# Kernel tuning notes

Measured on AMD Instinct MI355X. Metric: run time of the kernel, lower is better.

## Reference

```python
import jax, jax.numpy as jnp
import numpy as np


def setup_inputs() -> dict:
    key = jax.random.key(0)
    k1, k2 = jax.random.split(key)
    B, C, H, W = 16, 3, 512, 512
    predicted = jax.random.normal(k1, (B, C, H, W), dtype=jnp.float32)
    target = jax.random.randint(k2, (B, H, W), 0, 3, dtype=jnp.int32)
    return {"predicted": predicted, "target": target, "num_classes": 3}


def reference(predicted, target, num_classes):
    # predicted: [B, C, H, W] logits; target: [B, H, W] int labels
    B, C, H, W = predicted.shape
    smooth = 1.0

    # F.cross_entropy with default 'mean' reduction over all pixels
    logp = jax.nn.log_softmax(predicted, axis=1)           # [B,C,H,W]
    ce = -jnp.mean(jnp.take_along_axis(logp, target[:, None, :, :], axis=1))

    # Dice: the original casts softmax probs with .long() before summing,
    # which truncates toward zero (probs in [0,1) -> 0, exactly 1.0 -> 1).
    # We reproduce that faithfully with jnp.trunc.
    probs = jnp.exp(logp).reshape(B, C, H * W)             # softmax probs, [B,C,HW]
    tp = jnp.trunc(probs)                                   # faithful to .long() cast
    tgt = target.reshape(B, H * W)
    onehot = (tgt[:, None, :] == jnp.arange(num_classes)[None, :, None]).astype(probs.dtype)  # [B,nc,HW]

    intersection = jnp.sum(tp[:, :num_classes, :] * onehot, axis=-1)                 # [B,nc]
    union = jnp.sum(tp[:, :num_classes, :], axis=-1) + jnp.sum(onehot, axis=-1)      # [B,nc]
    coef = (2.0 * intersection + smooth) / (union + smooth)                           # [B,nc]
    batch_dice = jnp.mean(coef)  # mean over classes then batch == mean over both

    return ce + 1.0 - batch_dice
```

## Files before the change

kernel.cpp:

```cpp
#include <hip/hip_runtime.h>

constexpr int B_   = 16;
constexpr int C_   = 3;
constexpr int HW_  = 512 * 512;
constexpr int THREADS = 256;
constexpr int BLOCKS_PER_IMG = 128;
constexpr int NBLOCKS = B_ * BLOCKS_PER_IMG;
constexpr int F4_PER_BLOCK = HW_ / 4 / BLOCKS_PER_IMG;
constexpr int ITERS = F4_PER_BLOCK / THREADS;
constexpr int REC = 8;


__global__ __launch_bounds__(THREADS) void dice_ce_partial(
    const float* __restrict__ pred, const int* __restrict__ tgt,
    float* __restrict__ ws) {
  const int b = blockIdx.x / BLOCKS_PER_IMG;
  const int j = blockIdx.x % BLOCKS_PER_IMG;
  const int t = threadIdx.x;

  const float4* p0 = (const float4*)(pred + (size_t)b * C_ * HW_);
  const float4* p1 = (const float4*)(pred + (size_t)b * C_ * HW_ + HW_);
  const float4* p2 = (const float4*)(pred + (size_t)b * C_ * HW_ + 2 * HW_);
  const int4*   tg = (const int4*)(tgt + (size_t)b * HW_);

  float4 A0[ITERS], A1[ITERS], A2[ITERS];
  int4   T[ITERS];
#pragma unroll
  for (int i = 0; i < ITERS; ++i) {
    const int idx = j * F4_PER_BLOCK + i * THREADS + t;
    A0[i] = p0[idx];
    A1[i] = p1[idx];
    A2[i] = p2[idx];
    T[i]  = tg[idx];
  }

  float ce = 0.f;
  int pkA = 0, pkB = 0, pkC = 0, pkD = 0;

#pragma unroll
  for (int i = 0; i < ITERS; ++i) {
    float x0s[4] = {A0[i].x, A0[i].y, A0[i].z, A0[i].w};
    float x1s[4] = {A1[i].x, A1[i].y, A1[i].z, A1[i].w};
    float x2s[4] = {A2[i].x, A2[i].y, A2[i].z, A2[i].w};
    int   tvs[4] = {T[i].x, T[i].y, T[i].z, T[i].w};
#pragma unroll
    for (int k = 0; k < 4; ++k) {
      float x0 = x0s[k], x1 = x1s[k], x2 = x2s[k];
      int tv = tvs[k];
      float m  = fmaxf(x0, fmaxf(x1, x2));
      float e0 = __expf(x0 - m), e1 = __expf(x1 - m), e2 = __expf(x2 - m);
      float s  = e0 + e1 + e2;
      float ls = __logf(s);
      float xt = (tv == 0) ? x0 : ((tv == 1) ? x1 : x2);
      ce += (m + ls) - xt;
      int t0 = (e0 >= s) ? 1 : 0;
      int t1 = (e1 >= s) ? 1 : 0;
      int t2 = (e2 >= s) ? 1 : 0;
      pkA += ((tv == 1) ? 1 : 0) + ((tv == 2) ? (1 << 16) : 0);
      pkB += t0 + (t1 << 16);
      pkC += t2 + (((tv == 0) ? t0 : 0) << 16);
      pkD += ((tv == 1) ? t1 : 0) + (((tv == 2) ? t2 : 0) << 16);
    }
  }

  int pks[4] = {pkA, pkB, pkC, pkD};
#pragma unroll
  for (int off = 32; off > 0; off >>= 1) {
    ce += __shfl_down(ce, off, 64);
#pragma unroll
    for (int k = 0; k < 4; ++k) pks[k] += __shfl_down(pks[k], off, 64);
  }

  __shared__ float ceR[THREADS / 64];
  __shared__ int   pkR[THREADS / 64][4];
  const int wave = t >> 6, lane = t & 63;
  if (lane == 0) {
    ceR[wave] = ce;
#pragma unroll
    for (int k = 0; k < 4; ++k) pkR[wave][k] = pks[k];
  }
  __syncthreads();
  if (t == 0) {
#pragma unroll
    for (int w = 1; w < THREADS / 64; ++w) {
      ce += ceR[w];
#pragma unroll
      for (int k = 0; k < 4; ++k) pks[k] += pkR[w][k];
    }
    float4* rec = (float4*)(ws + (size_t)blockIdx.x * REC);
    rec[0] = make_float4(ce, __int_as_float(pks[0]), __int_as_float(pks[1]),
                         __int_as_float(pks[2]));
    rec[1] = make_float4(__int_as_float(pks[3]), 0.f, 0.f, 0.f);
  }
}

__global__ __launch_bounds__(1024) void dice_ce_final(
    const float* __restrict__ ws, float* __restrict__ out) {
  const int t = threadIdx.x;
  const int img = t >> 6;
  const int lane = t & 63;

  float ce = 0.f;
  float cnt1 = 0.f, cnt2 = 0.f;
  float tps0 = 0.f, tps1 = 0.f, tps2 = 0.f;
  float itr0 = 0.f, itr1 = 0.f, itr2 = 0.f;
#pragma unroll
  for (int r = 0; r < 2; ++r) {
    const int idx = img * BLOCKS_PER_IMG + r * 64 + lane;
    const float4* rec = (const float4*)(ws + (size_t)idx * REC);
    float4 r0 = rec[0], r1 = rec[1];
    ce += r0.x;
    int pA = __float_as_int(r0.y), pB = __float_as_int(r0.z);
    int pC = __float_as_int(r0.w), pD = __float_as_int(r1.x);
    cnt1 += (float)(pA & 0xffff); cnt2 += (float)(pA >> 16);
    tps0 += (float)(pB & 0xffff); tps1 += (float)(pB >> 16);
    tps2 += (float)(pC & 0xffff); itr0 += (float)(pC >> 16);
    itr1 += (float)(pD & 0xffff); itr2 += (float)(pD >> 16);
  }
  float v[9] = {ce, cnt1, cnt2, tps0, tps1, tps2, itr0, itr1, itr2};
#pragma unroll
  for (int k = 0; k < 9; ++k) {
#pragma unroll
    for (int off = 32; off > 0; off >>= 1) v[k] += __shfl_down(v[k], off, 64);
  }

  __shared__ float ceS[16];
  __shared__ float coefS[16];
  if (lane == 0) {
    float c1 = v[1], c2 = v[2];
    float c0 = (float)HW_ - c1 - c2;
    float coef = (2.f * v[6] + 1.f) / (v[3] + c0 + 1.f)
               + (2.f * v[7] + 1.f) / (v[4] + c1 + 1.f)
               + (2.f * v[8] + 1.f) / (v[5] + c2 + 1.f);
    ceS[img] = v[0];
    coefS[img] = coef;
  }
  __syncthreads();
  if (t == 0) {
    float cesum = 0.f, cf = 0.f;
#pragma unroll
    for (int i = 0; i < 16; ++i) { cesum += ceS[i]; cf += coefS[i]; }
    out[0] = cesum / ((float)B_ * (float)HW_) + 1.f - cf / (float)(B_ * C_);
  }
}

extern "C" void kernel_launch(void* const* d_in, const int* in_sizes, int n_in,
                              void* d_out, int out_size, void* d_ws, size_t ws_size,
                              hipStream_t stream) {
  const float* pred = (const float*)d_in[0];
  const int*   tgt  = (const int*)d_in[1];
  float*       out  = (float*)d_out;
  float*       ws   = (float*)d_ws;

  dice_ce_partial<<<NBLOCKS, THREADS, 0, stream>>>(pred, tgt, ws);
  dice_ce_final<<<1, 1024, 0, stream>>>(ws, out);
}
```

Baseline: 96.94 us.

## Fuse final reduction into partial kernel via last-block atomic counter

Replaces the separate single-block finalize kernel with a last-block-done pattern: each block publishes its record, fences, and increments a global counter, and the block that finishes last performs the cross-image reduction and writes the output. This removes one kernel launch and its gap but adds a hipMemsetAsync to reset the counter, an atomic per block, and a serial tail reduction done by only 256 threads. The memset is itself a stream operation, so the launch savings may be partly offset.

```diff
diff --git a/kernel.cpp b/kernel.cpp
--- a/kernel.cpp
+++ b/kernel.cpp
@@ -10,10 +10,11 @@
 constexpr int ITERS = F4_PER_BLOCK / THREADS;
 constexpr int REC = 8;
 
+constexpr size_t CNT_OFF_FLOATS = (size_t)NBLOCKS * REC;
 
-__global__ __launch_bounds__(THREADS) void dice_ce_partial(
+__global__ __launch_bounds__(THREADS) void dice_ce_fused(
     const float* __restrict__ pred, const int* __restrict__ tgt,
-    float* __restrict__ ws) {
+    float* __restrict__ ws, float* __restrict__ out) {
   const int b = blockIdx.x / BLOCKS_PER_IMG;
   const int j = blockIdx.x % BLOCKS_PER_IMG;
   const int t = threadIdx.x;
@@ -73,6 +74,9 @@
 
   __shared__ float ceR[THREADS / 64];
   __shared__ int   pkR[THREADS / 64][4];
+  __shared__ int   lastFlag;
+  __shared__ float ceS[B_];
+  __shared__ float coefS[B_];
   const int wave = t >> 6, lane = t & 63;
   if (lane == 0) {
     ceR[wave] = ce;
@@ -91,55 +95,58 @@
     rec[0] = make_float4(ce, __int_as_float(pks[0]), __int_as_float(pks[1]),
                          __int_as_float(pks[2]));
     rec[1] = make_float4(__int_as_float(pks[3]), 0.f, 0.f, 0.f);
+    __threadfence();
+    unsigned int old =
+        atomicAdd((unsigned int*)(ws + CNT_OFF_FLOATS), 1u);
+    lastFlag = (old == (unsigned int)(NBLOCKS - 1)) ? 1 : 0;
   }
-}
+  __syncthreads();
+  if (lastFlag == 0) return;
 
-__global__ __launch_bounds__(1024) void dice_ce_final(
-    const float* __restrict__ ws, float* __restrict__ out) {
-  const int t = threadIdx.x;
-  const int img = t >> 6;
-  const int lane = t & 63;
+  __threadfence();
 
-  float ce = 0.f;
-  float cnt1 = 0.f, cnt2 = 0.f;
-  float tps0 = 0.f, tps1 = 0.f, tps2 = 0.f;
-  float itr0 = 0.f, itr1 = 0.f, itr2 = 0.f;
 #pragma unroll
-  for (int r = 0; r < 2; ++r) {
-    const int idx = img * BLOCKS_PER_IMG + r * 64 + lane;
-    const float4* rec = (const float4*)(ws + (size_t)idx * REC);
-    float4 r0 = rec[0], r1 = rec[1];
-    ce += r0.x;
-    int pA = __float_as_int(r0.y), pB = __float_as_int(r0.z);
-    int pC = __float_as_int(r0.w), pD = __float_as_int(r1.x);
-    cnt1 += (float)(pA & 0xffff); cnt2 += (float)(pA >> 16);
-    tps0 += (float)(pB & 0xffff); tps1 += (float)(pB >> 16);
-    tps2 += (float)(pC & 0xffff); itr0 += (float)(pC >> 16);
-    itr1 += (float)(pD & 0xffff); itr2 += (float)(pD >> 16);
-  }
-  float v[9] = {ce, cnt1, cnt2, tps0, tps1, tps2, itr0, itr1, itr2};
+  for (int g = 0; g < 4; ++g) {
+    const int img = g * 4 + wave;
+    float ce2 = 0.f;
+    float cnt1 = 0.f, cnt2 = 0.f;
+    float tps0 = 0.f, tps1 = 0.f, tps2 = 0.f;
+    float itr0 = 0.f, itr1 = 0.f, itr2 = 0.f;
 #pragma unroll
-  for (int k = 0; k < 9; ++k) {
+    for (int r = 0; r < 2; ++r) {
+      const int idx = img * BLOCKS_PER_IMG + r * 64 + lane;
+      const float4* rec = (const float4*)(ws + (size_t)idx * REC);
+      float4 r0 = rec[0], r1 = rec[1];
+      ce2 += r0.x;
+      int pA = __float_as_int(r0.y), pB = __float_as_int(r0.z);
+      int pC = __float_as_int(r0.w), pD = __float_as_int(r1.x);
+      cnt1 += (float)(pA & 0xffff); cnt2 += (float)(pA >> 16);
+      tps0 += (float)(pB & 0xffff); tps1 += (float)(pB >> 16);
+      tps2 += (float)(pC & 0xffff); itr0 += (float)(pC >> 16);
+      itr1 += (float)(pD & 0xffff); itr2 += (float)(pD >> 16);
+    }
+    float v[9] = {ce2, cnt1, cnt2, tps0, tps1, tps2, itr0, itr1, itr2};
 #pragma unroll
-    for (int off = 32; off > 0; off >>= 1) v[k] += __shfl_down(v[k], off, 64);
-  }
-
-  __shared__ float ceS[16];
-  __shared__ float coefS[16];
-  if (lane == 0) {
-    float c1 = v[1], c2 = v[2];
-    float c0 = (float)HW_ - c1 - c2;
-    float coef = (2.f * v[6] + 1.f) / (v[3] + c0 + 1.f)
-               + (2.f * v[7] + 1.f) / (v[4] + c1 + 1.f)
-               + (2.f * v[8] + 1.f) / (v[5] + c2 + 1.f);
-    ceS[img] = v[0];
-    coefS[img] = coef;
+    for (int k = 0; k < 9; ++k) {
+#pragma unroll
+      for (int off = 32; off > 0; off >>= 1)
+        v[k] += __shfl_down(v[k], off, 64);
+    }
+    if (lane == 0) {
+      float c1 = v[1], c2 = v[2];
+      float c0 = (float)HW_ - c1 - c2;
+      float coef = (2.f * v[6] + 1.f) / (v[3] + c0 + 1.f)
+                 + (2.f * v[7] + 1.f) / (v[4] + c1 + 1.f)
+                 + (2.f * v[8] + 1.f) / (v[5] + c2 + 1.f);
+      ceS[img] = v[0];
+      coefS[img] = coef;
+    }
   }
   __syncthreads();
   if (t == 0) {
     float cesum = 0.f, cf = 0.f;
 #pragma unroll
-    for (int i = 0; i < 16; ++i) { cesum += ceS[i]; cf += coefS[i]; }
+    for (int i = 0; i < B_; ++i) { cesum += ceS[i]; cf += coefS[i]; }
     out[0] = cesum / ((float)B_ * (float)HW_) + 1.f - cf / (float)(B_ * C_);
   }
 }
@@ -152,6 +159,6 @@
   float*       out  = (float*)d_out;
   float*       ws   = (float*)d_ws;
 
-  dice_ce_partial<<<NBLOCKS, THREADS, 0, stream>>>(pred, tgt, ws);
-  dice_ce_final<<<1, 1024, 0, stream>>>(ws, out);
+  hipMemsetAsync((void*)(ws + CNT_OFF_FLOATS), 0, sizeof(unsigned int), stream);
+  dice_ce_fused<<<NBLOCKS, THREADS, 0, stream>>>(pred, tgt, ws, out);
 }
```

Result: slower. 157.7 us (+62.7%).

## Fuse final reduction into partial kernel via atomics and last-block tail

Applied to the files above, without the earlier changes.

Replaces the two-kernel scheme with a single kernel. Blocks atomically accumulate per-image packed counts and a fixed-point CE sum into device globals, and the last-arriving block computes the final loss and resets the accumulators. This removes the second launch and the workspace round trip. In exchange it adds global atomic contention and relies on self-resetting device state for correctness across calls.

```diff
diff --git a/kernel.cpp b/kernel.cpp
--- a/kernel.cpp
+++ b/kernel.cpp
@@ -8,12 +8,23 @@
 constexpr int NBLOCKS = B_ * BLOCKS_PER_IMG;
 constexpr int F4_PER_BLOCK = HW_ / 4 / BLOCKS_PER_IMG;
 constexpr int ITERS = F4_PER_BLOCK / THREADS;
-constexpr int REC = 8;
 
+constexpr float  CE_SCALE = 1048576.f;
+constexpr double CE_INV_D = 1.0 / 1048576.0;
 
-__global__ __launch_bounds__(THREADS) void dice_ce_partial(
+struct __align__(64) ImgAcc {
+  unsigned long long q[4];
+  unsigned long long ce;
+  unsigned arrive;
+  unsigned pad[5];
+};
+
+__device__ ImgAcc g_img[B_];
+__device__ unsigned g_done;
+
+__global__ __launch_bounds__(THREADS) void dice_ce_fused(
     const float* __restrict__ pred, const int* __restrict__ tgt,
-    float* __restrict__ ws) {
+    float* __restrict__ out) {
   const int b = blockIdx.x / BLOCKS_PER_IMG;
   const int j = blockIdx.x % BLOCKS_PER_IMG;
   const int t = threadIdx.x;
@@ -73,6 +84,7 @@
 
   __shared__ float ceR[THREADS / 64];
   __shared__ int   pkR[THREADS / 64][4];
+  __shared__ int   tailFlag;
   const int wave = t >> 6, lane = t & 63;
   if (lane == 0) {
     ceR[wave] = ce;
@@ -87,59 +99,64 @@
 #pragma unroll
       for (int k = 0; k < 4; ++k) pks[k] += pkR[w][k];
     }
-    float4* rec = (float4*)(ws + (size_t)blockIdx.x * REC);
-    rec[0] = make_float4(ce, __int_as_float(pks[0]), __int_as_float(pks[1]),
-                         __int_as_float(pks[2]));
-    rec[1] = make_float4(__int_as_float(pks[3]), 0.f, 0.f, 0.f);
+    ImgAcc* a = &g_img[b];
+    atomicAdd(&a->q[0], (unsigned long long)((unsigned)pks[0] & 0xffffu) |
+                        ((unsigned long long)((unsigned)pks[0] >> 16) << 32));
+    atomicAdd(&a->q[1], (unsigned long long)((unsigned)pks[1] & 0xffffu) |
+                        ((unsigned long long)((unsigned)pks[1] >> 16) << 32));
+    atomicAdd(&a->q[2], (unsigned long long)((unsigned)pks[2] & 0xffffu) |
+                        ((unsigned long long)((unsigned)pks[2] >> 16) << 32));
+    atomicAdd(&a->q[3], (unsigned long long)((unsigned)pks[3] & 0xffffu) |
+                        ((unsigned long long)((unsigned)pks[3] >> 16) << 32));
+    atomicAdd(&a->ce, (unsigned long long)llrintf(ce * CE_SCALE));
+    asm volatile("s_waitcnt vmcnt(0)" ::: "memory");
+    int tf = 0;
+    unsigned old = atomicAdd(&a->arrive, 1u);
+    if ((old & (unsigned)(BLOCKS_PER_IMG - 1)) == (unsigned)(BLOCKS_PER_IMG - 1)) {
+      unsigned od = atomicAdd(&g_done, 1u);
+      tf = ((od & (unsigned)(B_ - 1)) == (unsigned)(B_ - 1)) ? 1 : 0;
+    }
+    tailFlag = tf;
   }
-}
+  __syncthreads();
+  if (tailFlag == 0) return;
 
-__global__ __launch_bounds__(1024) void dice_ce_final(
-    const float* __restrict__ ws, float* __restrict__ out) {
-  const int t = threadIdx.x;
-  const int img = t >> 6;
-  const int lane = t & 63;
-
-  float ce = 0.f;
-  float cnt1 = 0.f, cnt2 = 0.f;
-  float tps0 = 0.f, tps1 = 0.f, tps2 = 0.f;
-  float itr0 = 0.f, itr1 = 0.f, itr2 = 0.f;
-#pragma unroll
-  for (int r = 0; r < 2; ++r) {
-    const int idx = img * BLOCKS_PER_IMG + r * 64 + lane;
-    const float4* rec = (const float4*)(ws + (size_t)idx * REC);
-    float4 r0 = rec[0], r1 = rec[1];
-    ce += r0.x;
-    int pA = __float_as_int(r0.y), pB = __float_as_int(r0.z);
-    int pC = __float_as_int(r0.w), pD = __float_as_int(r1.x);
-    cnt1 += (float)(pA & 0xffff); cnt2 += (float)(pA >> 16);
-    tps0 += (float)(pB & 0xffff); tps1 += (float)(pB >> 16);
-    tps2 += (float)(pC & 0xffff); itr0 += (float)(pC >> 16);
-    itr1 += (float)(pD & 0xffff); itr2 += (float)(pD >> 16);
-  }
-  float v[9] = {ce, cnt1, cnt2, tps0, tps1, tps2, itr0, itr1, itr2};
-#pragma unroll
-  for (int k = 0; k < 9; ++k) {
-#pragma unroll
-    for (int off = 32; off > 0; off >>= 1) v[k] += __shfl_down(v[k], off, 64);
-  }
-
-  __shared__ float ceS[16];
-  __shared__ float coefS[16];
-  if (lane == 0) {
-    float c1 = v[1], c2 = v[2];
-    float c0 = (float)HW_ - c1 - c2;
-    float coef = (2.f * v[6] + 1.f) / (v[3] + c0 + 1.f)
-               + (2.f * v[7] + 1.f) / (v[4] + c1 + 1.f)
-               + (2.f * v[8] + 1.f) / (v[5] + c2 + 1.f);
-    ceS[img] = v[0];
-    coefS[img] = coef;
+  __shared__ float coefS[B_];
+  __shared__ unsigned long long ceQ[B_];
+  if (t < B_) {
+    ImgAcc* a = &g_img[t];
+    unsigned long long q0 = __hip_atomic_load(&a->q[0], __ATOMIC_RELAXED, __HIP_MEMORY_SCOPE_AGENT);
+    unsigned long long q1 = __hip_atomic_load(&a->q[1], __ATOMIC_RELAXED, __HIP_MEMORY_SCOPE_AGENT);
+    unsigned long long q2 = __hip_atomic_load(&a->q[2], __ATOMIC_RELAXED, __HIP_MEMORY_SCOPE_AGENT);
+    unsigned long long q3 = __hip_atomic_load(&a->q[3], __ATOMIC_RELAXED, __HIP_MEMORY_SCOPE_AGENT);
+    unsigned long long cq = __hip_atomic_load(&a->ce,   __ATOMIC_RELAXED, __HIP_MEMORY_SCOPE_AGENT);
+    __hip_atomic_store(&a->q[0], 0ull, __ATOMIC_RELAXED, __HIP_MEMORY_SCOPE_AGENT);
+    __hip_atomic_store(&a->q[1], 0ull, __ATOMIC_RELAXED, __HIP_MEMORY_SCOPE_AGENT);
+    __hip_atomic_store(&a->q[2], 0ull, __ATOMIC_RELAXED, __HIP_MEMORY_SCOPE_AGENT);
+    __hip_atomic_store(&a->q[3], 0ull, __ATOMIC_RELAXED, __HIP_MEMORY_SCOPE_AGENT);
+    __hip_atomic_store(&a->ce,   0ull, __ATOMIC_RELAXED, __HIP_MEMORY_SCOPE_AGENT);
+    float cnt1 = (float)(unsigned)(q0 & 0xffffffffull);
+    float cnt2 = (float)(unsigned)(q0 >> 32);
+    float tps0 = (float)(unsigned)(q1 & 0xffffffffull);
+    float tps1 = (float)(unsigned)(q1 >> 32);
+    float tps2 = (float)(unsigned)(q2 & 0xffffffffull);
+    float itr0 = (float)(unsigned)(q2 >> 32);
+    float itr1 = (float)(unsigned)(q3 & 0xffffffffull);
+    float itr2 = (float)(unsigned)(q3 >> 32);
+    float c0 = (float)HW_ - cnt1 - cnt2;
+    float coef = (2.f * itr0 + 1.f) / (tps0 + c0 + 1.f)
+               + (2.f * itr1 + 1.f) / (tps1 + cnt1 + 1.f)
+               + (2.f * itr2 + 1.f) / (tps2 + cnt2 + 1.f);
+    coefS[t] = coef;
+    ceQ[t] = cq;
   }
   __syncthreads();
   if (t == 0) {
-    float cesum = 0.f, cf = 0.f;
+    unsigned long long tot = 0;
+    float cf = 0.f;
 #pragma unroll
-    for (int i = 0; i < 16; ++i) { cesum += ceS[i]; cf += coefS[i]; }
+    for (int i = 0; i < B_; ++i) { tot += ceQ[i]; cf += coefS[i]; }
+    float cesum = (float)((double)tot * CE_INV_D);
     out[0] = cesum / ((float)B_ * (float)HW_) + 1.f - cf / (float)(B_ * C_);
   }
 }
@@ -150,8 +167,7 @@
   const float* pred = (const float*)d_in[0];
   const int*   tgt  = (const int*)d_in[1];
   float*       out  = (float*)d_out;
-  float*       ws   = (float*)d_ws;
+  (void)d_ws; (void)ws_size;
 
-  dice_ce_partial<<<NBLOCKS, THREADS, 0, stream>>>(pred, tgt, ws);
-  dice_ce_final<<<1, 1024, 0, stream>>>(ws, out);
+  dice_ce_fused<<<NBLOCKS, THREADS, 0, stream>>>(pred, tgt, out);
 }
```

After: 112.1 us. 1.16x slower.
